# Optimization experiments

Hardware: AMD Instinct MI355X
Metric: run time of the kernel (lower is better)

The kernel has to match this reference:

```python
import jax, jax.numpy as jnp
import numpy as np

HALF = 16  # num_outputs // 2 with num_features = 32
EPS = 1e-5


def _gmul(Wm, h):
    # Wm: [B,N,M,J], h: [B,M,F] -> [B,N,J*F] (j-major feature layout, matching torch split/cat/bmm)
    B, N = Wm.shape[0], Wm.shape[1]
    return jnp.einsum('bnmj,bmf->bnjf', Wm, h).reshape(B, N, -1)


def _bn(z, g, b):
    # training-mode BatchNorm2d on [R, C, 1, 1] == per-channel norm over rows, biased var
    m = z.mean(axis=0)
    v = z.var(axis=0)
    return g * (z - m) / jnp.sqrt(v + EPS) + b


def _block(W, hx, W_lg, hy, P, wx2x, wy2x, bx, wy2y, wx2y, by, gx, btx, gy, bty):
    B, N, M = P.shape[0], P.shape[1], P.shape[2]
    x2x = _gmul(W, hx).reshape(-1, wx2x.shape[0])
    y2x = _gmul(P, hy).reshape(-1, wy2x.shape[0])
    zx = x2x @ wx2x + y2x @ wy2x + bx
    zx = jnp.concatenate([jax.nn.relu(zx[:, :HALF]), zx[:, HALF:]], axis=1)
    xo = _bn(zx, gx, btx).reshape(B, N, -1)
    y2y = _gmul(W_lg, hy).reshape(-1, wy2y.shape[0])
    x2y = _gmul(jnp.swapaxes(P, 1, 2), hx).reshape(-1, wx2y.shape[0])
    zy = y2y @ wy2y + x2y @ wx2y + by
    zy = jnp.concatenate([jax.nn.relu(zy[:, :HALF]), zy[:, HALF:]], axis=1)
    yo = _bn(zy, gy, bty).reshape(B, M, -1)
    return xo, yo


def _forward(W, x, W_lg, y, P,
             wx2x0, wy2x0, bx0, wy2y0, wx2y0, by0, gx0, btx0, gy0, bty0,
             wx2x_m, wy2x_m, bx_m, wy2y_m, wx2y_m, by_m, gx_m, btx_m, gy_m, bty_m,
             wlx, wly, bl):
    hx, hy = _block(W, x, W_lg, y, P, wx2x0, wy2x0, bx0, wy2y0, wx2y0, by0,
                    gx0, btx0, gy0, bty0)
    for i in range(wx2x_m.shape[0]):  # fixed num_layers loop
        hx, hy = _block(W, hx, W_lg, hy, P,
                        wx2x_m[i], wy2x_m[i], bx_m[i], wy2y_m[i], wx2y_m[i], by_m[i],
                        gx_m[i], btx_m[i], gy_m[i], bty_m[i])
    # final layer: linear only, x branch output
    x2x = _gmul(W, hx).reshape(-1, wlx.shape[0])
    y2x = _gmul(P, hy).reshape(-1, wly.shape[0])
    out = (x2x @ wlx + y2x @ wly + bl).reshape(W.shape[0], W.shape[1], -1)
    return out


def setup_inputs() -> dict:
    key = jax.random.key(0)
    ks = iter(jax.random.split(key, 40))
    B, N, M, J, F, L, C = 1, 2048, 4096, 3, 32, 6, 2
    d = {}
    d['W'] = jax.random.normal(next(ks), (B, N, N, J), jnp.float32)
    d['x'] = jax.random.normal(next(ks), (B, N, 1), jnp.float32)
    d['W_lg'] = jax.random.normal(next(ks), (B, M, M, J), jnp.float32)
    d['y'] = jax.random.normal(next(ks), (B, M, 1), jnp.float32)
    d['P'] = jax.random.normal(next(ks), (B, N, M, 2), jnp.float32)
    s = 0.1
    d['wx2x0'] = jax.random.normal(next(ks), (J * 1, F), jnp.float32) * s
    d['wy2x0'] = jax.random.normal(next(ks), (2 * 1, F), jnp.float32) * s
    d['bx0'] = jax.random.normal(next(ks), (F,), jnp.float32) * s
    d['wy2y0'] = jax.random.normal(next(ks), (J * 1, F), jnp.float32) * s
    d['wx2y0'] = jax.random.normal(next(ks), (2 * 1, F), jnp.float32) * s
    d['by0'] = jax.random.normal(next(ks), (F,), jnp.float32) * s
    d['gx0'] = jnp.ones((F,), jnp.float32)
    d['btx0'] = jnp.zeros((F,), jnp.float32)
    d['gy0'] = jnp.ones((F,), jnp.float32)
    d['bty0'] = jnp.zeros((F,), jnp.float32)
    d['wx2x_m'] = jax.random.normal(next(ks), (L, J * F, F), jnp.float32) * s
    d['wy2x_m'] = jax.random.normal(next(ks), (L, 2 * F, F), jnp.float32) * s
    d['bx_m'] = jax.random.normal(next(ks), (L, F), jnp.float32) * s
    d['wy2y_m'] = jax.random.normal(next(ks), (L, J * F, F), jnp.float32) * s
    d['wx2y_m'] = jax.random.normal(next(ks), (L, 2 * F, F), jnp.float32) * s
    d['by_m'] = jax.random.normal(next(ks), (L, F), jnp.float32) * s
    d['gx_m'] = jnp.ones((L, F), jnp.float32)
    d['btx_m'] = jnp.zeros((L, F), jnp.float32)
    d['gy_m'] = jnp.ones((L, F), jnp.float32)
    d['bty_m'] = jnp.zeros((L, F), jnp.float32)
    d['wlx'] = jax.random.normal(next(ks), (J * F, C), jnp.float32) * s
    d['wly'] = jax.random.normal(next(ks), (2 * F, C), jnp.float32) * s
    d['bl'] = jax.random.normal(next(ks), (C,), jnp.float32) * s
    return d


def reference(W, x, W_lg, y, P,
              wx2x0, wy2x0, bx0, wy2y0, wx2y0, by0, gx0, btx0, gy0, bty0,
              wx2x_m, wy2x_m, bx_m, wy2y_m, wx2y_m, by_m, gx_m, btx_m, gy_m, bty_m,
              wlx, wly, bl):
    return _forward(W, x, W_lg, y, P,
                    wx2x0, wy2x0, bx0, wy2y0, wx2y0, by0, gx0, btx0, gy0, bty0,
                    wx2x_m, wy2x_m, bx_m, wy2y_m, wx2y_m, by_m, gx_m, btx_m, gy_m, bty_m,
                    wlx, wly, bl)
```

## Files before the change

### kernel.cpp

```cpp
#include <hip/hip_runtime.h>

typedef _Float16 f16x8 __attribute__((ext_vector_type(8)));
typedef float f32x4 __attribute__((ext_vector_type(4)));
typedef unsigned short us4v __attribute__((ext_vector_type(4)));

__device__ inline unsigned short f16b(float v) {
    _Float16 h = (_Float16)v;
    return __builtin_bit_cast(unsigned short, h);
}

__device__ inline void atomAddF(float* p, float v) {
    __hip_atomic_fetch_add(p, v, __ATOMIC_RELAXED, __HIP_MEMORY_SCOPE_AGENT);
}

__global__ __launch_bounds__(256) void cvt_all(const float* __restrict__ W, const float* __restrict__ P,
                                               const float* __restrict__ WL,
                                               unsigned short* __restrict__ Wb, unsigned short* __restrict__ Pb,
                                               unsigned short* __restrict__ WLb) {
    int i = blockIdx.x * 256 + threadIdx.x;
    const float* src; unsigned short* dst; int idx;
    if (i < 3145728)               { src = W;  dst = Wb;  idx = i; }
    else if (i < 3145728 + 4194304){ src = P;  dst = Pb;  idx = i - 3145728; }
    else                           { src = WL; dst = WLb; idx = i - (3145728 + 4194304); }
    float4 v = ((const float4*)src)[idx];
    us4v o;
    o[0] = f16b(v.x); o[1] = f16b(v.y); o[2] = f16b(v.z); o[3] = f16b(v.w);
    ((us4v*)dst)[idx] = o;
}

__global__ __launch_bounds__(256) void transpose_p(const float* __restrict__ P,
                                                   unsigned short* __restrict__ PT) {
    __shared__ unsigned int lds[64][33];
    int bid = blockIdx.x;
    int m0 = (bid & 127) * 32;
    int n0 = (bid >> 7) * 64;
    int tid = threadIdx.x;
    const float2* P2 = (const float2*)P;
    #pragma unroll
    for (int it = 0; it < 8; ++it) {
        int idx = it * 256 + tid;
        int nl = idx >> 5, ml = idx & 31;
        float2 v = P2[(size_t)(n0 + nl) * 4096 + (m0 + ml)];
        unsigned int pk = (unsigned int)f16b(v.x) | ((unsigned int)f16b(v.y) << 16);
        lds[nl][ml] = pk;
    }
    __syncthreads();
    unsigned int* PTu = (unsigned int*)PT;
    #pragma unroll
    for (int it = 0; it < 8; ++it) {
        int idx = it * 256 + tid;
        int ml = idx >> 6, nl = idx & 63;
        PTu[(size_t)(m0 + ml) * 2048 + (n0 + nl)] = lds[nl][ml];
    }
}

__global__ __launch_bounds__(256) void build_b(
    const float* __restrict__ srcx, const float* __restrict__ srcy,
    int Fin, int Fout, int buildB2, int use_bn,
    const float* __restrict__ stats,
    const float* __restrict__ gx, const float* __restrict__ btx,
    const float* __restrict__ gy, const float* __restrict__ bty,
    const float* __restrict__ w1a, const float* __restrict__ w1b,
    const float* __restrict__ w2a, const float* __restrict__ w2b,
    unsigned short* __restrict__ B1f, unsigned short* __restrict__ B2f) {
    int tid0 = blockIdx.x * 256 + threadIdx.x;
    const int NB1 = 14336 * 32;
    int isB2 = 0, t2 = tid0;
    if (tid0 >= NB1) {
        if (!buildB2) return;
        isB2 = 1; t2 = tid0 - NB1;
        if (t2 >= 16384 * 32) return;
    }
    int e = t2 & 7, lane = (t2 >> 3) & 63, hh = (t2 >> 9) & 1, t = t2 >> 10;
    int k = (t << 5) | ((lane >> 4) << 3) | e;
    int g = (hh << 4) | (lane & 15);
    float v = 0.f;
    if (g < Fout) {
        const float* hr; const float* wc; int useY;
        if (!isB2) {
            if (k < 6144) { int m = k / 3, j = k - 3 * m; hr = srcx + m * Fin; wc = w1a + (j * Fin) * Fout + g; useY = 0; }
            else { int k2 = k - 6144; int m = k2 >> 1, p = k2 & 1; hr = srcy + m * Fin; wc = w1b + (p * Fin) * Fout + g; useY = 1; }
        } else {
            if (k < 12288) { int m = k / 3, j = k - 3 * m; hr = srcy + m * Fin; wc = w2a + (j * Fin) * Fout + g; useY = 1; }
            else { int k2 = k - 12288; int n = k2 >> 1, p = k2 & 1; hr = srcx + n * Fin; wc = w2b + (p * Fin) * Fout + g; useY = 0; }
        }
        float a = 0.f;
        if (use_bn) {
            const float* st = useY ? stats + 64 : stats;
            const float* gv = useY ? gy : gx;
            const float* bv = useY ? bty : btx;
            float invn = useY ? (1.f / 4096.f) : (1.f / 2048.f);
            #pragma unroll
            for (int f = 0; f < 32; ++f) {
                float mean = st[f] * invn;
                float var = st[32 + f] * invn - mean * mean;
                float sc = gv[f] * rsqrtf(var + 1e-5f);
                float h = sc * (hr[f] - mean) + bv[f];
                a += h * wc[f * Fout];
            }
        } else {
            for (int f = 0; f < Fin; ++f) a += hr[f] * wc[f * Fout];
        }
        v = a;
    }
    if (!isB2) B1f[t2] = f16b(v); else B2f[t2] = f16b(v);
}

__global__ __launch_bounds__(256) void gemm_k(
    const unsigned short* __restrict__ Wb, const unsigned short* __restrict__ Pb,
    const unsigned short* __restrict__ WLb, const unsigned short* __restrict__ PTb,
    const unsigned short* __restrict__ B1f, const unsigned short* __restrict__ B2f,
    float* __restrict__ px, float* __restrict__ py, float* __restrict__ stats, int nwgx) {
    __shared__ float lds[4][1024];
    int bid = blockIdx.x;
    if (bid == 0 && threadIdx.x < 128) stats[threadIdx.x] = 0.f;
    const unsigned short* Bf;
    float* Z;
    int seg, Mbase, rowlen, kloc, kb;
    const unsigned short* A16;
    if (bid < nwgx) {
        Bf = B1f;
        int mwg = bid / 14; seg = bid % 14;
        Mbase = mwg * 32;
        kb = seg << 10;
        Z = px + (size_t)seg * 65536;
        if (seg < 6) { rowlen = 6144; kloc = kb;        A16 = Wb; }
        else         { rowlen = 8192; kloc = kb - 6144; A16 = Pb; }
    } else {
        int b2 = bid - nwgx;
        Bf = B2f;
        int mwg = b2 / 16; seg = b2 % 16;
        Mbase = mwg * 32;
        kb = seg << 10;
        Z = py + (size_t)seg * 131072;
        if (seg < 12) { rowlen = 12288; kloc = kb;         A16 = WLb; }
        else          { rowlen = 4096;  kloc = kb - 12288; A16 = PTb; }
    }
    int wid = threadIdx.x >> 6, lane = threadIdx.x & 63;
    int kq = wid << 8;
    const unsigned short* ap0 = A16 + (size_t)(Mbase + (lane & 15)) * rowlen + kloc + kq + ((lane >> 4) << 3);
    const unsigned short* ap1 = ap0 + (size_t)16 * rowlen;
    const unsigned short* bp = Bf + ((size_t)((kb + kq) >> 5)) * 1024 + lane * 8;
    f32x4 acc00 = {0.f,0.f,0.f,0.f}, acc01 = {0.f,0.f,0.f,0.f};
    f32x4 acc10 = {0.f,0.f,0.f,0.f}, acc11 = {0.f,0.f,0.f,0.f};
    #pragma unroll
    for (int ks = 0; ks < 8; ++ks) {
        f16x8 a0 = *(const f16x8*)ap0;
        f16x8 a1 = *(const f16x8*)ap1;
        f16x8 b0 = *(const f16x8*)bp;
        f16x8 b1 = *(const f16x8*)(bp + 512);
        acc00 = __builtin_amdgcn_mfma_f32_16x16x32_f16(a0, b0, acc00, 0, 0, 0);
        acc10 = __builtin_amdgcn_mfma_f32_16x16x32_f16(a1, b0, acc10, 0, 0, 0);
        acc01 = __builtin_amdgcn_mfma_f32_16x16x32_f16(a0, b1, acc01, 0, 0, 0);
        acc11 = __builtin_amdgcn_mfma_f32_16x16x32_f16(a1, b1, acc11, 0, 0, 0);
        ap0 += 32; ap1 += 32; bp += 1024;
    }
    int col = lane & 15, r0 = (lane >> 4) << 2;
    float* l = lds[wid];
    #pragma unroll
    for (int r = 0; r < 4; ++r) {
        l[(r0 + r) * 32 + col]            = acc00[r];
        l[(r0 + r) * 32 + col + 16]       = acc01[r];
        l[(r0 + r + 16) * 32 + col]       = acc10[r];
        l[(r0 + r + 16) * 32 + col + 16]  = acc11[r];
    }
    __syncthreads();
    int t = threadIdx.x;
    float4 a = ((const float4*)lds[0])[t];
    float4 b = ((const float4*)lds[1])[t];
    float4 c = ((const float4*)lds[2])[t];
    float4 d = ((const float4*)lds[3])[t];
    float4 s;
    s.x = (a.x + b.x) + (c.x + d.x);
    s.y = (a.y + b.y) + (c.y + d.y);
    s.z = (a.z + b.z) + (c.z + d.z);
    s.w = (a.w + b.w) + (c.w + d.w);
    ((float4*)(Z + (size_t)Mbase * 32))[t] = s;
}

__global__ __launch_bounds__(256) void reduce_stats(
    const float* __restrict__ px, const float* __restrict__ py,
    const float* __restrict__ bx, const float* __restrict__ by,
    float* __restrict__ zax, float* __restrict__ zay,
    float* __restrict__ stats) {
    __shared__ float lsum[4][8][8];
    int bid = blockIdx.x, tid = threadIdx.x;
    const float4* src; const float* bias; float4* dst; float* st; int nseg, i4, stride4;
    if (bid < 64) { src = (const float4*)px; bias = bx; dst = (float4*)zax; st = stats;      nseg = 14; i4 = bid * 256 + tid;        stride4 = 16384; }
    else          { src = (const float4*)py; bias = by; dst = (float4*)zay; st = stats + 64; nseg = 16; i4 = (bid - 64) * 256 + tid; stride4 = 32768; }
    float4 s = {0.f, 0.f, 0.f, 0.f};
    for (int g = 0; g < nseg; ++g) {
        float4 v = src[(size_t)g * stride4 + i4];
        s.x += v.x; s.y += v.y; s.z += v.z; s.w += v.w;
    }
    int c0 = (i4 & 7) * 4;
    float4 b4 = *(const float4*)(bias + c0);
    s.x += b4.x; s.y += b4.y; s.z += b4.z; s.w += b4.w;
    if (c0 < 16) {
        s.x = fmaxf(s.x, 0.f); s.y = fmaxf(s.y, 0.f);
        s.z = fmaxf(s.z, 0.f); s.w = fmaxf(s.w, 0.f);
    }
    dst[i4] = s;
    float4 s2 = {s.x * s.x, s.y * s.y, s.z * s.z, s.w * s.w};
    #pragma unroll
    for (int mask = 8; mask <= 32; mask <<= 1) {
        s.x += __shfl_xor(s.x, mask); s.y += __shfl_xor(s.y, mask);
        s.z += __shfl_xor(s.z, mask); s.w += __shfl_xor(s.w, mask);
        s2.x += __shfl_xor(s2.x, mask); s2.y += __shfl_xor(s2.y, mask);
        s2.z += __shfl_xor(s2.z, mask); s2.w += __shfl_xor(s2.w, mask);
    }
    int w = tid >> 6, ln = tid & 63;
    if (ln < 8) {
        lsum[w][ln][0] = s.x;  lsum[w][ln][1] = s.y;  lsum[w][ln][2] = s.z;  lsum[w][ln][3] = s.w;
        lsum[w][ln][4] = s2.x; lsum[w][ln][5] = s2.y; lsum[w][ln][6] = s2.z; lsum[w][ln][7] = s2.w;
    }
    __syncthreads();
    if (tid < 64) {
        int q = tid >> 3, e = tid & 7;
        float v = lsum[0][q][e] + lsum[1][q][e] + lsum[2][q][e] + lsum[3][q][e];
        int col = q * 4 + (e & 3);
        atomAddF((e < 4) ? &st[col] : &st[32 + col], v);
    }
}

__global__ __launch_bounds__(256) void out_final(const float* __restrict__ px,
                                                 const float* __restrict__ bl,
                                                 float* __restrict__ out) {
    int tid = blockIdx.x * 256 + threadIdx.x;
    if (tid < 4096) {
        int n = tid >> 1, c = tid & 1;
        float a = bl[c];
        for (int s = 0; s < 14; ++s) a += px[(size_t)s * 65536 + n * 32 + c];
        out[tid] = a;
    }
}

extern "C" void kernel_launch(void* const* d_in, const int* in_sizes, int n_in,
                              void* d_out, int out_size, void* d_ws, size_t ws_size,
                              hipStream_t stream) {
    const float* W    = (const float*)d_in[0];
    const float* x    = (const float*)d_in[1];
    const float* WL   = (const float*)d_in[2];
    const float* y    = (const float*)d_in[3];
    const float* P    = (const float*)d_in[4];
    const float* wx2x0 = (const float*)d_in[5];
    const float* wy2x0 = (const float*)d_in[6];
    const float* bx0   = (const float*)d_in[7];
    const float* wy2y0 = (const float*)d_in[8];
    const float* wx2y0 = (const float*)d_in[9];
    const float* by0   = (const float*)d_in[10];
    const float* gx0   = (const float*)d_in[11];
    const float* btx0  = (const float*)d_in[12];
    const float* gy0   = (const float*)d_in[13];
    const float* bty0  = (const float*)d_in[14];
    const float* wx2x_m = (const float*)d_in[15];
    const float* wy2x_m = (const float*)d_in[16];
    const float* bx_m   = (const float*)d_in[17];
    const float* wy2y_m = (const float*)d_in[18];
    const float* wx2y_m = (const float*)d_in[19];
    const float* by_m   = (const float*)d_in[20];
    const float* gx_m   = (const float*)d_in[21];
    const float* btx_m  = (const float*)d_in[22];
    const float* gy_m   = (const float*)d_in[23];
    const float* bty_m  = (const float*)d_in[24];
    const float* wlx = (const float*)d_in[25];
    const float* wly = (const float*)d_in[26];
    const float* bl  = (const float*)d_in[27];

    char* base = (char*)d_ws;
    unsigned short* Wb  = (unsigned short*)(base + 0);
    unsigned short* Pb  = (unsigned short*)(base + 25165824);
    unsigned short* WLb = (unsigned short*)(base + 58720256);
    unsigned short* PTb = (unsigned short*)(base + 159383552);
    unsigned short* B1f = (unsigned short*)(base + 192937984);
    unsigned short* B2f = (unsigned short*)(base + 193855488);
    float* zax   = (float*)(base + 194904064);
    float* zay   = (float*)(base + 195166208);
    float* stats = (float*)(base + 195690496);
    float* px    = (float*)(base + 195691008);
    float* py    = (float*)(base + 199361024);

    cvt_all<<<77824, 256, 0, stream>>>(W, P, WL, Wb, Pb, WLb);
    transpose_p<<<4096, 256, 0, stream>>>(P, PTb);

    build_b<<<3840, 256, 0, stream>>>(x, y, 1, 32, 1, 0, nullptr, nullptr, nullptr, nullptr, nullptr,
                                      wx2x0, wy2x0, wy2y0, wx2y0, B1f, B2f);
    gemm_k<<<2944, 256, 0, stream>>>(Wb, Pb, WLb, PTb, B1f, B2f, px, py, stats, 896);
    reduce_stats<<<192, 256, 0, stream>>>(px, py, bx0, by0, zax, zay, stats);

    for (int i = 0; i < 6; ++i) {
        const float* gv  = (i == 0) ? gx0  : gx_m  + (i - 1) * 32;
        const float* bv  = (i == 0) ? btx0 : btx_m + (i - 1) * 32;
        const float* gvy = (i == 0) ? gy0  : gy_m  + (i - 1) * 32;
        const float* bvy = (i == 0) ? bty0 : bty_m + (i - 1) * 32;
        build_b<<<3840, 256, 0, stream>>>(zax, zay, 32, 32, 1, 1, stats, gv, bv, gvy, bvy,
                                          wx2x_m + i * 3072, wy2x_m + i * 2048,
                                          wy2y_m + i * 3072, wx2y_m + i * 2048, B1f, B2f);
        gemm_k<<<2944, 256, 0, stream>>>(Wb, Pb, WLb, PTb, B1f, B2f, px, py, stats, 896);
        reduce_stats<<<192, 256, 0, stream>>>(px, py, bx_m + i * 32, by_m + i * 32, zax, zay, stats);
    }

    build_b<<<1792, 256, 0, stream>>>(zax, zay, 32, 2, 0, 1, stats,
                                      gx_m + 5 * 32, btx_m + 5 * 32, gy_m + 5 * 32, bty_m + 5 * 32,
                                      wlx, wly, nullptr, nullptr, B1f, B2f);
    gemm_k<<<896, 256, 0, stream>>>(Wb, Pb, WLb, PTb, B1f, B2f, px, py, stats, 896);
    out_final<<<16, 256, 0, stream>>>(px, bl, (float*)d_out);
}
```

Measured before the change: 707.8 us.

## Pack f16 adjacency matrices into MFMA-fragment panel layout for contiguous loads

The f32-to-f16 conversion kernel now writes W, P and W_lg (and the transposed P) in a panel-major layout: 16-row panels with 32-wide k-steps arranged so each wavefront's MFMA A-fragment load is one contiguous 1 KB chunk. The GEMM kernel's A pointers are rewritten to walk this layout, so per-lane loads become fully coalesced instead of 16 strided row segments. The one-time conversion now reads rows with a scattered pattern and writes coalesced, and the transpose kernel's stores become scattered. The point is to make the seven repeated GEMM passes cheaper at the cost of a slower one-time preprocessing step.

```diff
diff --git a/kernel.cpp b/kernel.cpp
--- a/kernel.cpp
+++ b/kernel.cpp
@@ -2,7 +2,7 @@
 
 typedef _Float16 f16x8 __attribute__((ext_vector_type(8)));
 typedef float f32x4 __attribute__((ext_vector_type(4)));
-typedef unsigned short us4v __attribute__((ext_vector_type(4)));
+
 
 __device__ inline unsigned short f16b(float v) {
     _Float16 h = (_Float16)v;
@@ -13,19 +13,35 @@
     __hip_atomic_fetch_add(p, v, __ATOMIC_RELAXED, __HIP_MEMORY_SCOPE_AGENT);
 }
 
-__global__ __launch_bounds__(256) void cvt_all(const float* __restrict__ W, const float* __restrict__ P,
-                                               const float* __restrict__ WL,
-                                               unsigned short* __restrict__ Wb, unsigned short* __restrict__ Pb,
-                                               unsigned short* __restrict__ WLb) {
-    int i = blockIdx.x * 256 + threadIdx.x;
-    const float* src; unsigned short* dst; int idx;
-    if (i < 3145728)               { src = W;  dst = Wb;  idx = i; }
-    else if (i < 3145728 + 4194304){ src = P;  dst = Pb;  idx = i - 3145728; }
-    else                           { src = WL; dst = WLb; idx = i - (3145728 + 4194304); }
-    float4 v = ((const float4*)src)[idx];
-    us4v o;
-    o[0] = f16b(v.x); o[1] = f16b(v.y); o[2] = f16b(v.z); o[3] = f16b(v.w);
-    ((us4v*)dst)[idx] = o;
+template<int K>
+__device__ inline void pack_cvt(const float* __restrict__ src, unsigned short* __restrict__ dst, int u) {
+    int o = u * 8;
+    int panel = o / (K * 16);
+    int rem = o - panel * (K * 16);
+    int kstep = rem >> 9;
+    int rem2 = rem & 511;
+    int g = rem2 >> 7;
+    int r15 = (rem2 >> 3) & 15;
+    int row = (panel << 4) | r15;
+    int k = (kstep << 5) | (g << 3);
+    const float4* s = (const float4*)(src + (size_t)row * K + k);
+    float4 v0 = s[0], v1 = s[1];
+    uint4 q;
+    q.x = (unsigned)f16b(v0.x) | ((unsigned)f16b(v0.y) << 16);
+    q.y = (unsigned)f16b(v0.z) | ((unsigned)f16b(v0.w) << 16);
+    q.z = (unsigned)f16b(v1.x) | ((unsigned)f16b(v1.y) << 16);
+    q.w = (unsigned)f16b(v1.z) | ((unsigned)f16b(v1.w) << 16);
+    ((uint4*)dst)[u] = q;
+}
+
+__global__ __launch_bounds__(256) void cvt_pack(const float* __restrict__ W, const float* __restrict__ P,
+                                                const float* __restrict__ WL,
+                                                unsigned short* __restrict__ Wb, unsigned short* __restrict__ Pb,
+                                                unsigned short* __restrict__ WLb) {
+    int u = blockIdx.x * 256 + threadIdx.x;
+    if (u < 1572864) pack_cvt<6144>(W, Wb, u);
+    else if (u < 1572864 + 2097152) pack_cvt<8192>(P, Pb, u - 1572864);
+    else pack_cvt<12288>(WL, WLb, u - (1572864 + 2097152));
 }
 
 __global__ __launch_bounds__(256) void transpose_p(const float* __restrict__ P,
@@ -50,7 +66,10 @@
     for (int it = 0; it < 8; ++it) {
         int idx = it * 256 + tid;
         int ml = idx >> 6, nl = idx & 63;
-        PTu[(size_t)(m0 + ml) * 2048 + (n0 + nl)] = lds[nl][ml];
+        int row = m0 + ml;
+        int k2 = (n0 + nl) * 2;
+        int o = ((row >> 4) << 16) | ((k2 >> 5) << 9) | (((((k2 >> 3) & 3) << 4) | (row & 15)) << 3) | (k2 & 7);
+        PTu[o >> 1] = lds[nl][ml];
     }
 }
 
@@ -116,7 +135,7 @@
     if (bid == 0 && threadIdx.x < 128) stats[threadIdx.x] = 0.f;
     const unsigned short* Bf;
     float* Z;
-    int seg, Mbase, rowlen, kloc, kb;
+    int seg, Mbase, K, kloc, kb;
     const unsigned short* A16;
     if (bid < nwgx) {
         Bf = B1f;
@@ -124,8 +143,8 @@
         Mbase = mwg * 32;
         kb = seg << 10;
         Z = px + (size_t)seg * 65536;
-        if (seg < 6) { rowlen = 6144; kloc = kb;        A16 = Wb; }
-        else         { rowlen = 8192; kloc = kb - 6144; A16 = Pb; }
+        if (seg < 6) { K = 6144; kloc = kb;        A16 = Wb; }
+        else         { K = 8192; kloc = kb - 6144; A16 = Pb; }
     } else {
         int b2 = bid - nwgx;
         Bf = B2f;
@@ -133,13 +152,14 @@
         Mbase = mwg * 32;
         kb = seg << 10;
         Z = py + (size_t)seg * 131072;
-        if (seg < 12) { rowlen = 12288; kloc = kb;         A16 = WLb; }
-        else          { rowlen = 4096;  kloc = kb - 12288; A16 = PTb; }
+        if (seg < 12) { K = 12288; kloc = kb;         A16 = WLb; }
+        else          { K = 4096;  kloc = kb - 12288; A16 = PTb; }
     }
     int wid = threadIdx.x >> 6, lane = threadIdx.x & 63;
     int kq = wid << 8;
-    const unsigned short* ap0 = A16 + (size_t)(Mbase + (lane & 15)) * rowlen + kloc + kq + ((lane >> 4) << 3);
-    const unsigned short* ap1 = ap0 + (size_t)16 * rowlen;
+    const unsigned short* ap0 = A16 + (size_t)(Mbase >> 4) * (K * 16)
+                              + (size_t)((kloc + kq) >> 5) * 512 + lane * 8;
+    const unsigned short* ap1 = ap0 + (size_t)K * 16;
     const unsigned short* bp = Bf + ((size_t)((kb + kq) >> 5)) * 1024 + lane * 8;
     f32x4 acc00 = {0.f,0.f,0.f,0.f}, acc01 = {0.f,0.f,0.f,0.f};
     f32x4 acc10 = {0.f,0.f,0.f,0.f}, acc11 = {0.f,0.f,0.f,0.f};
@@ -153,7 +173,7 @@
         acc10 = __builtin_amdgcn_mfma_f32_16x16x32_f16(a1, b0, acc10, 0, 0, 0);
         acc01 = __builtin_amdgcn_mfma_f32_16x16x32_f16(a0, b1, acc01, 0, 0, 0);
         acc11 = __builtin_amdgcn_mfma_f32_16x16x32_f16(a1, b1, acc11, 0, 0, 0);
-        ap0 += 32; ap1 += 32; bp += 1024;
+        ap0 += 512; ap1 += 512; bp += 1024;
     }
     int col = lane & 15, r0 = (lane >> 4) << 2;
     float* l = lds[wid];
@@ -280,7 +300,7 @@
     float* px    = (float*)(base + 195691008);
     float* py    = (float*)(base + 199361024);
 
-    cvt_all<<<77824, 256, 0, stream>>>(W, P, WL, Wb, Pb, WLb);
+    cvt_pack<<<38912, 256, 0, stream>>>(W, P, WL, Wb, Pb, WLb);
     transpose_p<<<4096, 256, 0, stream>>>(P, PTb);
 
     build_b<<<3840, 256, 0, stream>>>(x, y, 1, 32, 1, 0, nullptr, nullptr, nullptr, nullptr, nullptr,
```

New measurement: 683.1 us. 3.5% less time.
